# Kernel optimization log

Measured on AMD Instinct MI355X. Metric: run time of the kernel, lower is better.

Reference implementation:

```python
import jax, jax.numpy as jnp
import numpy as np

RADIUS = 0.2
NSAMPLE = 32
USE_XYZ = True

B, N, S, C = 8, 8192, 2048, 64


def setup_inputs() -> dict:
    key = jax.random.key(0)
    k1, k2, k3 = jax.random.split(key, 3)
    xyz = jax.random.uniform(k1, (B, N, 3), dtype=jnp.float32)
    new_xyz = jax.random.uniform(k2, (B, S, 3), dtype=jnp.float32)
    features = jax.random.normal(k3, (B, N, C), dtype=jnp.float32)
    return {"xyz": xyz, "new_xyz": new_xyz, "features": features}


def _ball_query(new_xyz, xyz, radius, nsample):
    # new_xyz: (B,S,3), xyz: (B,N,3) -> idx (B,S,nsample) int32
    n = xyz.shape[1]
    d2 = jnp.sum((new_xyz[:, :, None, :] - xyz[:, None, :, :]) ** 2, axis=-1)  # (B,S,N)
    mask = d2 < radius * radius
    # keys: index j if inside ball else N (sentinel); smallest nsample keys = first
    # nsample in-ball indices in ascending j order (matches CUDA ball_query order).
    keys = jnp.where(mask, jnp.arange(n, dtype=jnp.int32), jnp.int32(n))
    neg_vals, _ = jax.lax.top_k(-keys, nsample)  # top_k of -keys -> smallest keys
    idx = -neg_vals  # (B,S,nsample), ascending
    first = idx[..., 0:1]
    idx = jnp.where(idx == n, first, idx)   # pad empty slots with first hit
    idx = jnp.where(idx == n, 0, idx)       # balls with zero hits -> index 0
    return idx


def _group(points, idx):
    # points: (B,N,D), idx: (B,S,K) -> (B,S,K,D)
    return jax.vmap(lambda p, i: p[i])(points, idx)


def reference(xyz, new_xyz, features):
    idx = _ball_query(new_xyz, xyz, RADIUS, NSAMPLE)
    grouped_xyz = _group(xyz, idx) - new_xyz[:, :, None, :]  # (B,S,K,3)
    grouped_feat = _group(features, idx)                      # (B,S,K,C)
    if USE_XYZ:
        new_features = jnp.concatenate([grouped_xyz, grouped_feat], axis=-1)
    else:
        new_features = grouped_feat
    return jnp.transpose(new_features, (0, 3, 1, 2))  # (B, C+3, S, K)
```

## Files before the change

### kernel.cpp

```cpp
#include <hip/hip_runtime.h>

#define BB 8
#define NN 8192
#define SS 2048
#define CC 64
#define NS 32
#define COUT 67
#define QT 4
#define SLOTS (QT*NS)
#define FSTR 65

__global__ __launch_bounds__(256) void fused_kernel(
    const float* __restrict__ xyz,
    const float* __restrict__ new_xyz,
    const float* __restrict__ feat,
    float* __restrict__ out)
{
#pragma clang fp contract(off)
    __shared__ float ft[SLOTS * FSTR];
    __shared__ float xt[3 * SLOTS];
    __shared__ int idx_sh[SLOTS];

    const int t   = threadIdx.x;
    const int w   = t >> 6;
    const int ln  = t & 63;
    const int bid = blockIdx.x;
    const int b     = bid & 7;
    const int sTile = bid >> 3;
    const int s0 = sTile * QT;

    {
        const int s = s0 + w;
        const float R2 = 0.04f;

        const float* ctr = new_xyz + ((size_t)b * SS + s) * 3;
        const float cx = ctr[0], cy = ctr[1], cz = ctr[2];
        const float* xb = xyz + (size_t)b * NN * 3;

        int* myidx = idx_sh + (w << 5);
        const unsigned long long lt = (1ull << ln) - 1ull;

        int total = 0;
        int firstIdx = -1;
        for (int j0 = 0; j0 < NN && total < NS; j0 += 256) {
            const float4* p4 = (const float4*)(xb + (size_t)(j0 + (ln << 2)) * 3);
            const float4 A  = p4[0];
            const float4 Bv = p4[1];
            const float4 Cv = p4[2];
            float d2v[4];
            {
                const float dx = A.x - cx, dy = A.y - cy, dz = A.z - cz;
                float d2 = dx * dx; d2 = d2 + dy * dy; d2 = d2 + dz * dz;
                d2v[0] = d2;
            }
            {
                const float dx = A.w - cx, dy = Bv.x - cy, dz = Bv.y - cz;
                float d2 = dx * dx; d2 = d2 + dy * dy; d2 = d2 + dz * dz;
                d2v[1] = d2;
            }
            {
                const float dx = Bv.z - cx, dy = Bv.w - cy, dz = Cv.x - cz;
                float d2 = dx * dx; d2 = d2 + dy * dy; d2 = d2 + dz * dz;
                d2v[2] = d2;
            }
            {
                const float dx = Cv.y - cx, dy = Cv.z - cy, dz = Cv.w - cz;
                float d2 = dx * dx; d2 = d2 + dy * dy; d2 = d2 + dz * dz;
                d2v[3] = d2;
            }

            unsigned long long M[4];
#pragma unroll
            for (int u = 0; u < 4; ++u) M[u] = __ballot(d2v[u] < R2);

            if (firstIdx < 0) {
                int fmin = 0x7fffffff;
#pragma unroll
                for (int u = 0; u < 4; ++u)
                    if (M[u] != 0ull) {
                        const int j = j0 + (__builtin_ctzll(M[u]) << 2) + u;
                        fmin = (j < fmin) ? j : fmin;
                    }
                if (fmin != 0x7fffffff) firstIdx = fmin;
            }

            int below = 0;
#pragma unroll
            for (int u = 0; u < 4; ++u) below += (int)__popcll(M[u] & lt);

            int own = 0;
#pragma unroll
            for (int u = 0; u < 4; ++u) {
                if (d2v[u] < R2) {
                    const int pos = total + below + own;
                    if (pos < NS) myidx[pos] = j0 + (ln << 2) + u;
                    ++own;
                }
            }
#pragma unroll
            for (int u = 0; u < 4; ++u) total += (int)__popcll(M[u]);
        }
        if (total < NS) {
            const int fill = (total > 0) ? firstIdx : 0;
            if (ln >= total && ln < NS) myidx[ln] = fill;
        }
    }
    __syncthreads();

    if (t < SLOTS) {
        const int r = idx_sh[t];
        const int q = t >> 5;
        const float* ctr = new_xyz + ((size_t)b * SS + s0 + q) * 3;
        const float* p   = xyz + ((size_t)b * NN + r) * 3;
        xt[0 * SLOTS + t] = p[0] - ctr[0];
        xt[1 * SLOTS + t] = p[1] - ctr[1];
        xt[2 * SLOTS + t] = p[2] - ctr[2];
    }

    const float* fb = feat + (size_t)b * NN * CC;
    for (int i = 0; i < 32; i += 4) {
        float v[4];
        int   mm[4];
#pragma unroll
        for (int u = 0; u < 4; ++u) {
            const int m = (w << 5) + i + u;
            mm[u] = m;
            v[u]  = fb[(size_t)idx_sh[m] * CC + ln];
        }
#pragma unroll
        for (int u = 0; u < 4; ++u)
            ft[mm[u] * FSTR + ln] = v[u];
    }
    __syncthreads();

    const size_t plane = (size_t)SS * NS;
    float* ob = out + ((size_t)b * COUT * SS + s0) * NS;
    for (int i = 0; i < 34; ++i) {
        const int tau = (i << 2) + w;
        if (tau < 134) {
            const int p  = tau >> 1;
            const int j  = tau & 1;
            const int sl = (j << 6) + ln;
            const float val = (p < 3) ? xt[p * SLOTS + sl]
                                      : ft[sl * FSTR + (p - 3)];
            ob[(size_t)p * plane + sl] = val;
        }
    }
}

extern "C" void kernel_launch(void* const* d_in, const int* in_sizes, int n_in,
                              void* d_out, int out_size, void* d_ws, size_t ws_size,
                              hipStream_t stream) {
    const float* xyz     = (const float*)d_in[0];
    const float* new_xyz = (const float*)d_in[1];
    const float* feat    = (const float*)d_in[2];
    float* out = (float*)d_out;
    (void)d_ws; (void)ws_size;

    fused_kernel<<<dim3((BB * SS) / QT), dim3(256), 0, stream>>>(xyz, new_xyz, feat, out);
}
```

Baseline: 179.1 us.

## Stage features through half-size LDS tile in two passes to raise occupancy

The per-block feature staging buffer is halved: the 64 feature channels are gathered and transposed in two passes of 32 channels, each followed by a write-out phase. Launch bounds now request 6 blocks per CU. Shared memory drops from about 35KB to about 19KB, so more blocks can reside per CU to hide gather latency. In exchange there are extra __syncthreads barriers, and each half-row gather reads only 128 bytes per point.

```diff
diff --git a/kernel.cpp b/kernel.cpp
--- a/kernel.cpp
+++ b/kernel.cpp
@@ -8,16 +8,16 @@
 #define COUT 67
 #define QT 4
 #define SLOTS (QT*NS)
-#define FSTR 65
+#define HSTR 33
 
-__global__ __launch_bounds__(256) void fused_kernel(
+__global__ __launch_bounds__(256, 6) void fused_kernel(
     const float* __restrict__ xyz,
     const float* __restrict__ new_xyz,
     const float* __restrict__ feat,
     float* __restrict__ out)
 {
 #pragma clang fp contract(off)
-    __shared__ float ft[SLOTS * FSTR];
+    __shared__ float fh[SLOTS * HSTR];
     __shared__ float xt[3 * SLOTS];
     __shared__ int idx_sh[SLOTS];
 
@@ -117,34 +117,59 @@
         xt[2 * SLOTS + t] = p[2] - ctr[2];
     }
 
+    const int c32 = ln & 31;
+    const int sub = ln >> 5;
     const float* fb = feat + (size_t)b * NN * CC;
-    for (int i = 0; i < 32; i += 4) {
+    const size_t plane = (size_t)SS * NS;
+    float* ob = out + ((size_t)b * COUT * SS + s0) * NS;
+
+    for (int i = 0; i < 16; i += 4) {
         float v[4];
         int   mm[4];
 #pragma unroll
         for (int u = 0; u < 4; ++u) {
-            const int m = (w << 5) + i + u;
+            const int m = (w << 5) + ((i + u) << 1) + sub;
             mm[u] = m;
-            v[u]  = fb[(size_t)idx_sh[m] * CC + ln];
+            v[u]  = fb[(size_t)idx_sh[m] * CC + c32];
         }
 #pragma unroll
         for (int u = 0; u < 4; ++u)
-            ft[mm[u] * FSTR + ln] = v[u];
+            fh[mm[u] * HSTR + c32] = v[u];
     }
     __syncthreads();
 
-    const size_t plane = (size_t)SS * NS;
-    float* ob = out + ((size_t)b * COUT * SS + s0) * NS;
-    for (int i = 0; i < 34; ++i) {
+    for (int i = 0; i < 18; ++i) {
         const int tau = (i << 2) + w;
-        if (tau < 134) {
+        if (tau < 70) {
             const int p  = tau >> 1;
-            const int j  = tau & 1;
-            const int sl = (j << 6) + ln;
+            const int sl = ((tau & 1) << 6) + ln;
             const float val = (p < 3) ? xt[p * SLOTS + sl]
-                                      : ft[sl * FSTR + (p - 3)];
+                                      : fh[sl * HSTR + (p - 3)];
             ob[(size_t)p * plane + sl] = val;
         }
+    }
+    __syncthreads();
+
+    for (int i = 0; i < 16; i += 4) {
+        float v[4];
+        int   mm[4];
+#pragma unroll
+        for (int u = 0; u < 4; ++u) {
+            const int m = (w << 5) + ((i + u) << 1) + sub;
+            mm[u] = m;
+            v[u]  = fb[(size_t)idx_sh[m] * CC + 32 + c32];
+        }
+#pragma unroll
+        for (int u = 0; u < 4; ++u)
+            fh[mm[u] * HSTR + c32] = v[u];
+    }
+    __syncthreads();
+
+    for (int i = 0; i < 16; ++i) {
+        const int tau = (i << 2) + w;
+        const int pl  = tau >> 1;
+        const int sl  = ((tau & 1) << 6) + ln;
+        ob[(size_t)(35 + pl) * plane + sl] = fh[sl * HSTR + pl];
     }
 }
 
```

After: 176.9 us. About the same (-1.3%).

## Process 8 queries per block with float4 gathers and channel-staged vectorized stores

Applied to the files above, without the earlier changes.

Doubles the queries per block to 8 (two ball-query passes per wave), so each block writes 256 contiguous floats per output channel plane. Feature gathers become float4 loads, transposed into a channel-major shared buffer one 16-channel stage at a time. That buffer is then written back with float4 global stores. The aim is wider, more coalesced global traffic and a smaller shared-memory footprint, so more blocks fit per CU. In exchange each block does twice the serial ball-query work and adds extra syncs between stages.

```diff
diff --git a/kernel.cpp b/kernel.cpp
--- a/kernel.cpp
+++ b/kernel.cpp
@@ -6,19 +6,19 @@
 #define CC 64
 #define NS 32
 #define COUT 67
-#define QT 4
+#define QT 8
 #define SLOTS (QT*NS)
-#define FSTR 65
+#define SP 260
 
-__global__ __launch_bounds__(256) void fused_kernel(
+__global__ __launch_bounds__(256, 6) void fused_kernel(
     const float* __restrict__ xyz,
     const float* __restrict__ new_xyz,
     const float* __restrict__ feat,
     float* __restrict__ out)
 {
 #pragma clang fp contract(off)
-    __shared__ float ft[SLOTS * FSTR];
-    __shared__ float xt[3 * SLOTS];
+    __shared__ float fh[16 * SP];
+    __shared__ float xt[3 * SP];
     __shared__ int idx_sh[SLOTS];
 
     const int t   = threadIdx.x;
@@ -29,15 +29,16 @@
     const int sTile = bid >> 3;
     const int s0 = sTile * QT;
 
-    {
-        const int s = s0 + w;
+    for (int qi = 0; qi < 2; ++qi) {
+        const int q = (qi << 2) + w;
+        const int s = s0 + q;
         const float R2 = 0.04f;
 
         const float* ctr = new_xyz + ((size_t)b * SS + s) * 3;
         const float cx = ctr[0], cy = ctr[1], cz = ctr[2];
         const float* xb = xyz + (size_t)b * NN * 3;
 
-        int* myidx = idx_sh + (w << 5);
+        int* myidx = idx_sh + (q << 5);
         const unsigned long long lt = (1ull << ln) - 1ull;
 
         int total = 0;
@@ -107,43 +108,61 @@
     }
     __syncthreads();
 
-    if (t < SLOTS) {
+    const int c4  = ln & 3;
+    const int ms  = ln >> 2;
+    const float* fb = feat + (size_t)b * NN * CC;
+    const size_t plane = (size_t)SS * NS;
+    float* ob = out + ((size_t)b * COUT * SS + s0) * NS;
+
+    {
         const int r = idx_sh[t];
         const int q = t >> 5;
         const float* ctr = new_xyz + ((size_t)b * SS + s0 + q) * 3;
         const float* p   = xyz + ((size_t)b * NN + r) * 3;
-        xt[0 * SLOTS + t] = p[0] - ctr[0];
-        xt[1 * SLOTS + t] = p[1] - ctr[1];
-        xt[2 * SLOTS + t] = p[2] - ctr[2];
+        xt[0 * SP + t] = p[0] - ctr[0];
+        xt[1 * SP + t] = p[1] - ctr[1];
+        xt[2 * SP + t] = p[2] - ctr[2];
     }
 
-    const float* fb = feat + (size_t)b * NN * CC;
-    for (int i = 0; i < 32; i += 4) {
-        float v[4];
-        int   mm[4];
 #pragma unroll
-        for (int u = 0; u < 4; ++u) {
-            const int m = (w << 5) + i + u;
-            mm[u] = m;
-            v[u]  = fb[(size_t)idx_sh[m] * CC + ln];
+    for (int st = 0; st < 4; ++st) {
+        if (st > 0) __syncthreads();
+
+        float4 vv[4];
+        int    mm[4];
+#pragma unroll
+        for (int i = 0; i < 4; ++i) {
+            mm[i] = (w << 6) + (i << 4) + ms;
+            vv[i] = *(const float4*)(fb + (size_t)idx_sh[mm[i]] * CC
+                                     + (st << 4) + (c4 << 2));
         }
 #pragma unroll
-        for (int u = 0; u < 4; ++u)
-            ft[mm[u] * FSTR + ln] = v[u];
-    }
-    __syncthreads();
+        for (int i = 0; i < 4; ++i) {
+            fh[((c4 << 2) + 0) * SP + mm[i]] = vv[i].x;
+            fh[((c4 << 2) + 1) * SP + mm[i]] = vv[i].y;
+            fh[((c4 << 2) + 2) * SP + mm[i]] = vv[i].z;
+            fh[((c4 << 2) + 3) * SP + mm[i]] = vv[i].w;
+        }
+        __syncthreads();
 
-    const size_t plane = (size_t)SS * NS;
-    float* ob = out + ((size_t)b * COUT * SS + s0) * NS;
-    for (int i = 0; i < 34; ++i) {
-        const int tau = (i << 2) + w;
-        if (tau < 134) {
-            const int p  = tau >> 1;
-            const int j  = tau & 1;
-            const int sl = (j << 6) + ln;
-            const float val = (p < 3) ? xt[p * SLOTS + sl]
-                                      : ft[sl * FSTR + (p - 3)];
-            ob[(size_t)p * plane + sl] = val;
+        if (st == 0) {
+            for (int i = 0; i < 5; ++i) {
+                const int tau = (i << 2) + w;
+                if (tau < 19) {
+                    const float* src = (tau < 3) ? (xt + tau * SP)
+                                                 : (fh + (tau - 3) * SP);
+                    const float4 v = *(const float4*)(src + (ln << 2));
+                    *(float4*)(ob + (size_t)tau * plane + (ln << 2)) = v;
+                }
+            }
+        } else {
+#pragma unroll
+            for (int i = 0; i < 4; ++i) {
+                const int tau = (i << 2) + w;
+                const float4 v = *(const float4*)(fh + tau * SP + (ln << 2));
+                *(float4*)(ob + (size_t)(3 + (st << 4) + tau) * plane
+                           + (ln << 2)) = v;
+            }
         }
     }
 }
```

Result: faster. 175.5 us (-2.0%).

## Process eight queries per block, overlapping second-half ball query with first-half gather

Applied to the files above, without the earlier changes.

Each block now handles eight query points in two halves of four. The ball-query scan for the second half is interleaved in chunks with the staged feature gather and output stores of the first half, so compute overlaps memory traffic. Features are gathered with float4 loads, staged through a smaller 16-channel shared tile, and written out as float4 stores; a min-blocks-per-SM launch bound is also added to raise occupancy. The cost is more barriers and more complex control flow, and the extra scan chunks can stall the gather when a query needs many chunks.

```diff
diff --git a/kernel.cpp b/kernel.cpp
--- a/kernel.cpp
+++ b/kernel.cpp
@@ -6,20 +6,19 @@
 #define CC 64
 #define NS 32
 #define COUT 67
-#define QT 4
-#define SLOTS (QT*NS)
-#define FSTR 65
-
-__global__ __launch_bounds__(256) void fused_kernel(
+#define QT 8
+#define SPA 132
+
+__global__ __launch_bounds__(256, 6) void fused_kernel(
     const float* __restrict__ xyz,
     const float* __restrict__ new_xyz,
     const float* __restrict__ feat,
     float* __restrict__ out)
 {
 #pragma clang fp contract(off)
-    __shared__ float ft[SLOTS * FSTR];
-    __shared__ float xt[3 * SLOTS];
-    __shared__ int idx_sh[SLOTS];
+    __shared__ float fh[16 * SPA];
+    __shared__ float xt[3 * SPA];
+    __shared__ int idx_sh[256];
 
     const int t   = threadIdx.x;
     const int w   = t >> 6;
@@ -29,45 +28,27 @@
     const int sTile = bid >> 3;
     const int s0 = sTile * QT;
 
-    {
-        const int s = s0 + w;
-        const float R2 = 0.04f;
-
-        const float* ctr = new_xyz + ((size_t)b * SS + s) * 3;
-        const float cx = ctr[0], cy = ctr[1], cz = ctr[2];
-        const float* xb = xyz + (size_t)b * NN * 3;
-
-        int* myidx = idx_sh + (w << 5);
-        const unsigned long long lt = (1ull << ln) - 1ull;
-
-        int total = 0;
-        int firstIdx = -1;
-        for (int j0 = 0; j0 < NN && total < NS; j0 += 256) {
+    const float R2 = 0.04f;
+    const float* xb = xyz + (size_t)b * NN * 3;
+    const unsigned long long lt = (1ull << ln) - 1ull;
+
+    auto scan_chunks = [&](float cx, float cy, float cz, int* myidx,
+                           int& j0r, int& total, int& firstIdx, int maxc) {
+        for (int c = 0; c < maxc && j0r < NN && total < NS; ++c) {
+            const int j0 = j0r;
             const float4* p4 = (const float4*)(xb + (size_t)(j0 + (ln << 2)) * 3);
             const float4 A  = p4[0];
             const float4 Bv = p4[1];
             const float4 Cv = p4[2];
             float d2v[4];
-            {
-                const float dx = A.x - cx, dy = A.y - cy, dz = A.z - cz;
-                float d2 = dx * dx; d2 = d2 + dy * dy; d2 = d2 + dz * dz;
-                d2v[0] = d2;
-            }
-            {
-                const float dx = A.w - cx, dy = Bv.x - cy, dz = Bv.y - cz;
-                float d2 = dx * dx; d2 = d2 + dy * dy; d2 = d2 + dz * dz;
-                d2v[1] = d2;
-            }
-            {
-                const float dx = Bv.z - cx, dy = Bv.w - cy, dz = Cv.x - cz;
-                float d2 = dx * dx; d2 = d2 + dy * dy; d2 = d2 + dz * dz;
-                d2v[2] = d2;
-            }
-            {
-                const float dx = Cv.y - cx, dy = Cv.z - cy, dz = Cv.w - cz;
-                float d2 = dx * dx; d2 = d2 + dy * dy; d2 = d2 + dz * dz;
-                d2v[3] = d2;
-            }
+            { const float dx = A.x - cx, dy = A.y - cy, dz = A.z - cz;
+              float d2 = dx * dx; d2 = d2 + dy * dy; d2 = d2 + dz * dz; d2v[0] = d2; }
+            { const float dx = A.w - cx, dy = Bv.x - cy, dz = Bv.y - cz;
+              float d2 = dx * dx; d2 = d2 + dy * dy; d2 = d2 + dz * dz; d2v[1] = d2; }
+            { const float dx = Bv.z - cx, dy = Bv.w - cy, dz = Cv.x - cz;
+              float d2 = dx * dx; d2 = d2 + dy * dy; d2 = d2 + dz * dz; d2v[2] = d2; }
+            { const float dx = Cv.y - cx, dy = Cv.z - cy, dz = Cv.w - cz;
+              float d2 = dx * dx; d2 = d2 + dy * dy; d2 = d2 + dz * dz; d2v[3] = d2; }
 
             unsigned long long M[4];
 #pragma unroll
@@ -99,52 +80,123 @@
             }
 #pragma unroll
             for (int u = 0; u < 4; ++u) total += (int)__popcll(M[u]);
+            j0r += 256;
         }
-        if (total < NS) {
-            const int fill = (total > 0) ? firstIdx : 0;
-            if (ln >= total && ln < NS) myidx[ln] = fill;
+    };
+
+    {
+        const float* ctrA = new_xyz + ((size_t)b * SS + s0 + w) * 3;
+        int jA = 0, totA = 0, fA = -1;
+        scan_chunks(ctrA[0], ctrA[1], ctrA[2], idx_sh + (w << 5),
+                    jA, totA, fA, 32);
+        if (totA < NS) {
+            const int fill = (totA > 0) ? fA : 0;
+            if (ln >= totA && ln < NS) idx_sh[(w << 5) + ln] = fill;
         }
     }
     __syncthreads();
 
-    if (t < SLOTS) {
+    const float* ctrB = new_xyz + ((size_t)b * SS + s0 + 4 + w) * 3;
+    const float cbx = ctrB[0], cby = ctrB[1], cbz = ctrB[2];
+    int jB = 0, totB = 0, fB = -1;
+    int* myidxB = idx_sh + 128 + (w << 5);
+
+    if (t < 128) {
         const int r = idx_sh[t];
         const int q = t >> 5;
         const float* ctr = new_xyz + ((size_t)b * SS + s0 + q) * 3;
-        const float* p   = xyz + ((size_t)b * NN + r) * 3;
-        xt[0 * SLOTS + t] = p[0] - ctr[0];
-        xt[1 * SLOTS + t] = p[1] - ctr[1];
-        xt[2 * SLOTS + t] = p[2] - ctr[2];
+        const float* p   = xb + (size_t)r * 3;
+        xt[0 * SPA + t] = p[0] - ctr[0];
+        xt[1 * SPA + t] = p[1] - ctr[1];
+        xt[2 * SPA + t] = p[2] - ctr[2];
     }
 
     const float* fb = feat + (size_t)b * NN * CC;
-    for (int i = 0; i < 32; i += 4) {
-        float v[4];
-        int   mm[4];
-#pragma unroll
-        for (int u = 0; u < 4; ++u) {
-            const int m = (w << 5) + i + u;
-            mm[u] = m;
-            v[u]  = fb[(size_t)idx_sh[m] * CC + ln];
-        }
-#pragma unroll
-        for (int u = 0; u < 4; ++u)
-            ft[mm[u] * FSTR + ln] = v[u];
-    }
-    __syncthreads();
-
     const size_t plane = (size_t)SS * NS;
     float* ob = out + ((size_t)b * COUT * SS + s0) * NS;
-    for (int i = 0; i < 34; ++i) {
-        const int tau = (i << 2) + w;
-        if (tau < 134) {
-            const int p  = tau >> 1;
-            const int j  = tau & 1;
-            const int sl = (j << 6) + ln;
-            const float val = (p < 3) ? xt[p * SLOTS + sl]
-                                      : ft[sl * FSTR + (p - 3)];
-            ob[(size_t)p * plane + sl] = val;
+
+    const int m  = t >> 1;
+    const int fq = t & 1;
+    const int cb = fq << 3;
+    const float* frowA = fb + (size_t)idx_sh[m] * CC + (fq << 3);
+
+    auto store_stage = [&](int st, int soff) {
+        const int ofs = (ln & 31) << 2;
+        if (st == 0) {
+            for (int i = 0; i < 3; ++i) {
+                const int tt = (i << 2) + w;
+                if (tt < 10) {
+                    const int p = (tt << 1) + (ln >> 5);
+                    if (p < 19) {
+                        const float* src = (p < 3) ? (xt + p * SPA)
+                                                   : (fh + (p - 3) * SPA);
+                        const float4 v = *(const float4*)(src + ofs);
+                        *(float4*)(ob + (size_t)p * plane + soff + ofs) = v;
+                    }
+                }
+            }
+        } else {
+            for (int i = 0; i < 2; ++i) {
+                const int tt = (i << 2) + w;
+                const int j  = (tt << 1) + (ln >> 5);
+                const float4 v = *(const float4*)(fh + j * SPA + ofs);
+                *(float4*)(ob + (size_t)(3 + (st << 4) + j) * plane
+                           + soff + ofs) = v;
+            }
         }
+    };
+
+#pragma unroll
+    for (int st = 0; st < 4; ++st) {
+        const float4 v0 = *(const float4*)(frowA + (st << 4));
+        const float4 v1 = *(const float4*)(frowA + (st << 4) + 4);
+        scan_chunks(cbx, cby, cbz, myidxB, jB, totB, fB, 4);
+        __syncthreads();
+        fh[(cb + 0) * SPA + m] = v0.x;
+        fh[(cb + 1) * SPA + m] = v0.y;
+        fh[(cb + 2) * SPA + m] = v0.z;
+        fh[(cb + 3) * SPA + m] = v0.w;
+        fh[(cb + 4) * SPA + m] = v1.x;
+        fh[(cb + 5) * SPA + m] = v1.y;
+        fh[(cb + 6) * SPA + m] = v1.z;
+        fh[(cb + 7) * SPA + m] = v1.w;
+        __syncthreads();
+        store_stage(st, 0);
+    }
+
+    scan_chunks(cbx, cby, cbz, myidxB, jB, totB, fB, 32);
+    if (totB < NS) {
+        const int fill = (totB > 0) ? fB : 0;
+        if (ln >= totB && ln < NS) myidxB[ln] = fill;
+    }
+    __syncthreads();
+
+    if (t < 128) {
+        const int r = idx_sh[128 + t];
+        const int q = 4 + (t >> 5);
+        const float* ctr = new_xyz + ((size_t)b * SS + s0 + q) * 3;
+        const float* p   = xb + (size_t)r * 3;
+        xt[0 * SPA + t] = p[0] - ctr[0];
+        xt[1 * SPA + t] = p[1] - ctr[1];
+        xt[2 * SPA + t] = p[2] - ctr[2];
+    }
+    const float* frowB = fb + (size_t)idx_sh[128 + m] * CC + (fq << 3);
+
+#pragma unroll
+    for (int st = 0; st < 4; ++st) {
+        const float4 v0 = *(const float4*)(frowB + (st << 4));
+        const float4 v1 = *(const float4*)(frowB + (st << 4) + 4);
+        __syncthreads();
+        fh[(cb + 0) * SPA + m] = v0.x;
+        fh[(cb + 1) * SPA + m] = v0.y;
+        fh[(cb + 2) * SPA + m] = v0.z;
+        fh[(cb + 3) * SPA + m] = v0.w;
+        fh[(cb + 4) * SPA + m] = v1.x;
+        fh[(cb + 5) * SPA + m] = v1.y;
+        fh[(cb + 6) * SPA + m] = v1.z;
+        fh[(cb + 7) * SPA + m] = v1.w;
+        __syncthreads();
+        store_stage(st, 128);
     }
 }
 
```

Result: no change. 176.2 us (-1.6%).
